# Kernel optimization log

Hardware: AMD Instinct MI355X
Metric: run time of the kernel (lower is better)

The kernel has to match this reference:

```python
import jax, jax.numpy as jnp
import numpy as np

B, S, E, H = 2, 2048, 2048, 16
D = E // H

def setup_inputs() -> dict:
    key = jax.random.key(0)
    ks = jax.random.split(key, 9)
    sc = 1.0 / np.sqrt(E)
    return {
        "x":  jax.random.normal(ks[0], (B, S, E), jnp.float32),
        "Wq": jax.random.normal(ks[1], (E, E), jnp.float32) * sc,
        "bq": jax.random.normal(ks[2], (E,), jnp.float32) * 0.01,
        "Wk": jax.random.normal(ks[3], (E, E), jnp.float32) * sc,
        "bk": jax.random.normal(ks[4], (E,), jnp.float32) * 0.01,
        "Wv": jax.random.normal(ks[5], (E, E), jnp.float32) * sc,
        "bv": jax.random.normal(ks[6], (E,), jnp.float32) * 0.01,
        "Wo": jax.random.normal(ks[7], (E, E), jnp.float32) * sc,
        "bo": jax.random.normal(ks[8], (E,), jnp.float32) * 0.01,
    }

def _split_heads(t):
    # [B,S,E] -> [B,H,S,D]
    return t.reshape(B, S, H, D).transpose(0, 2, 1, 3)

def reference(x, Wq, bq, Wk, bk, Wv, bv, Wo, bo):
    # projections (nn.Linear: y = x @ W^T + b)
    q = _split_heads(x @ Wq.T + bq)
    k = _split_heads(x @ Wk.T + bk)
    v = _split_heads(x @ Wv.T + bv)

    # scaled causal attention; scale uses k.size(-1) == head_dim D
    scores = jnp.einsum("bhqd,bhkd->bhqk", q, k) / jnp.sqrt(jnp.asarray(D, q.dtype))
    causal = jnp.tril(jnp.ones((S, S), bool))  # [S,S]
    scores = jnp.where(causal[None, None, :, :], scores, -jnp.inf)
    # training path subtracts row max before softmax (no-op under stable softmax)
    scores = scores - jnp.max(scores, axis=-1, keepdims=True)
    attn = jax.nn.softmax(scores, axis=-1)
    # dropout_rate = 0.0 -> identity
    ctx = jnp.einsum("bhqk,bhkd->bhqd", attn, v)

    # merge heads [B,H,S,D] -> [B,S,E], final projection
    out = ctx.transpose(0, 2, 1, 3).reshape(B, S, E)
    return out @ Wo.T + bo
```

## Files before the change

kernel.cpp:

```cpp
#include <hip/hip_runtime.h>

typedef unsigned short u16;
typedef __attribute__((ext_vector_type(4))) float f32x4;
typedef __attribute__((ext_vector_type(8))) short s16x8;
typedef __attribute__((ext_vector_type(4))) unsigned short u16x4;
typedef __attribute__((ext_vector_type(2))) unsigned u32x2;

#define MFMA16(a, b, c) __builtin_amdgcn_mfma_f32_16x16x32_bf16((a), (b), (c), 0, 0, 0)

__device__ __forceinline__ u16 f2bf(float f) {
  union { float f; unsigned u; } v; v.f = f;
  unsigned u = v.u;
  u += 0x7fffu + ((u >> 16) & 1u);
  return (u16)(u >> 16);
}

__device__ __forceinline__ unsigned cvtpk(float a, float b) {
  unsigned r;
  asm("v_cvt_pk_bf16_f32 %0, %1, %2" : "=v"(r) : "v"(a), "v"(b));
  return r;
}

__device__ __forceinline__ void gl_lds16(const void* g, void* l) {
  __builtin_amdgcn_global_load_lds(
      (const __attribute__((address_space(1))) void*)g,
      (__attribute__((address_space(3))) void*)l, 16, 0, 0);
}

__global__ void cast6(const float* __restrict__ x,
                      const float* __restrict__ w0, const float* __restrict__ w1,
                      const float* __restrict__ w2, const float* __restrict__ w3,
                      u16* __restrict__ ws) {
  const int y = blockIdx.y;
  const float* src;
  u16* dst;
  if (y < 2) { src = x + (size_t)y * 4194304; dst = ws + (size_t)y * 4194304; }
  else {
    src = (y == 2) ? w0 : (y == 3) ? w1 : (y == 4) ? w2 : w3;
    dst = ws + 8388608 + (size_t)(y - 2) * 4194304;
  }
  const int i = blockIdx.x * 256 + threadIdx.x;
  f32x4 v = ((const f32x4*)src)[i];
  u16x4 o;
#pragma unroll
  for (int e = 0; e < 4; ++e) o[e] = f2bf(v[e]);
  ((u16x4*)dst)[i] = o;
}

template <int SWAP>
__device__ __forceinline__ void gemm_core(const u16* __restrict__ A,
                                          const u16* __restrict__ Bw,
                                          u16* sA, u16* sB,
                                          f32x4 (&acc)[4][4],
                                          int m0, int n0, int tid) {
  const int lane = tid & 63, w = tid >> 6;
  const int ln = lane & 15, quad = lane >> 4, ln7 = ln & 7;
  const int wm = (w >> 1) * 64, wn = (w & 1) * 64;
  const int srow = lane >> 3;
  const int scol = (((lane & 7) ^ srow)) * 8;

  for (int k0 = 0; k0 < 2048; k0 += 64) {
#pragma unroll
    for (int c = 0; c < 4; ++c) {
      const int chunk = c * 4 + w;
      const int row = chunk * 8 + srow;
      gl_lds16(A + (size_t)(m0 + row) * 2048 + k0 + scol, (char*)sA + chunk * 1024);
      gl_lds16(Bw + (size_t)(n0 + row) * 2048 + k0 + scol, (char*)sB + chunk * 1024);
    }
    __syncthreads();
#pragma unroll
    for (int kk = 0; kk < 64; kk += 32) {
      s16x8 af[4], bf[4];
      const int g = (kk >> 3) + quad;
#pragma unroll
      for (int t = 0; t < 4; ++t) {
        af[t] = *(const s16x8*)&sA[(wm + t * 16 + ln) * 64 + ((g ^ ln7) << 3)];
        bf[t] = *(const s16x8*)&sB[(wn + t * 16 + ln) * 64 + ((g ^ ln7) << 3)];
      }
#pragma unroll
      for (int tm = 0; tm < 4; ++tm)
#pragma unroll
        for (int tn = 0; tn < 4; ++tn)
          acc[tm][tn] = SWAP ? MFMA16(bf[tn], af[tm], acc[tm][tn])
                             : MFMA16(af[tm], bf[tn], acc[tm][tn]);
    }
    __syncthreads();
  }
}

__global__ __launch_bounds__(512, 2) void gemm_qk256(
    const u16* __restrict__ A,
    const u16* __restrict__ W0, const u16* __restrict__ W1,
    const float* __restrict__ b0, const float* __restrict__ b1,
    u16* __restrict__ Qo, u16* __restrict__ Ko) {
  __shared__ __align__(16) u16 smem[65536];
  const int z = blockIdx.z;
  const u16* Bw = z ? W1 : W0;
  const float* bias = z ? b1 : b0;
  u16* out = z ? Ko : Qo;
  const float scale = z ? 1.0f : 0.1275174306003988f;

  const int tid = threadIdx.x;
  const int lane = tid & 63, w = tid >> 6;
  const int ln = lane & 15, quad = lane >> 4, ln7 = lane & 7;
  const int m0 = blockIdx.y * 256, n0 = blockIdx.x * 256;
  const int wm = (w >> 2) << 7, wn = (w & 3) << 6;

  const int ci0 = tid, ci1 = 512 + tid;
  const int r0 = ci0 >> 3, c0k = ((ci0 & 7) ^ (r0 & 7)) << 3;
  const int r1 = ci1 >> 3, c1k = ((ci1 & 7) ^ (r1 & 7)) << 3;
  const int abase = (w >> 2) << 13;
  const int bbase = 16384 + (((w >> 1) & 1) << 13) + ((w & 1) << 12);
  const int sw0 = (quad ^ ln7) << 3, sw1 = ((4 + quad) ^ ln7) << 3;

  f32x4 acc[8][4] = {};
  s16x8 af[8][2], bf[4][2];

  auto STGA = [&](int t) {
    u16* dst = smem + ((t & 1) << 15);
    const int kc = (t & 31) << 6;
    const u16* s0 = A + (size_t)(m0 + r0) * 2048 + kc + c0k;
    const u16* s1 = A + (size_t)(m0 + r1) * 2048 + kc + c1k;
    gl_lds16(s0, dst + ci0 * 8);
    gl_lds16(s1, dst + ci1 * 8);
    gl_lds16(s0 + (size_t)128 * 2048, dst + 8192 + ci0 * 8);
    gl_lds16(s1 + (size_t)128 * 2048, dst + 8192 + ci1 * 8);
  };
  auto STGB = [&](int t) {
    u16* dst = smem + ((t & 1) << 15) + 16384;
    const int kc = (t & 31) << 6;
    const u16* s0 = Bw + (size_t)(n0 + r0) * 2048 + kc + c0k;
    const u16* s1 = Bw + (size_t)(n0 + r1) * 2048 + kc + c1k;
    gl_lds16(s0, dst + ci0 * 8);
    gl_lds16(s1, dst + ci1 * 8);
    gl_lds16(s0 + (size_t)128 * 2048, dst + 8192 + ci0 * 8);
    gl_lds16(s1 + (size_t)128 * 2048, dst + 8192 + ci1 * 8);
  };
  auto RDA = [&](int buf, int tm0) {
    const u16* p = smem + (buf << 15) + abase;
#pragma unroll
    for (int u = 0; u < 4; ++u) {
      const int tt = tm0 + u;
      af[tt][0] = *(const s16x8*)&p[(tt * 16 + ln) * 64 + sw0];
      af[tt][1] = *(const s16x8*)&p[(tt * 16 + ln) * 64 + sw1];
    }
  };
  auto RDB = [&](int buf, int tn0) {
    const u16* p = smem + (buf << 15) + bbase;
#pragma unroll
    for (int u = 0; u < 2; ++u) {
      const int tt = tn0 + u;
      bf[tt][0] = *(const s16x8*)&p[(tt * 16 + ln) * 64 + sw0];
      bf[tt][1] = *(const s16x8*)&p[(tt * 16 + ln) * 64 + sw1];
    }
  };
  auto QM = [&](int tm0, int tn0) {
    __builtin_amdgcn_s_setprio(1);
#pragma unroll
    for (int tm = tm0; tm < tm0 + 4; ++tm)
#pragma unroll
      for (int tn = tn0; tn < tn0 + 2; ++tn)
#pragma unroll
        for (int ks = 0; ks < 2; ++ks)
          acc[tm][tn] = MFMA16(bf[tn][ks], af[tm][ks], acc[tm][tn]);
    __builtin_amdgcn_s_setprio(0);
  };

#define BAR()                                   \
  asm volatile("" ::: "memory");                \
  __builtin_amdgcn_s_barrier();                 \
  asm volatile("" ::: "memory")
#define SEAL() asm volatile("s_waitcnt vmcnt(0)" ::: "memory")

  STGA(0); STGB(0); STGA(1);
  asm volatile("s_waitcnt vmcnt(4)" ::: "memory");
  BAR();
  RDA(0, 0); RDB(0, 0);

#pragma unroll 1
  for (int u = 0; u < 16; ++u) {
    const int t = 2 * u;
    QM(0, 0);
    RDA(0, 4);
    STGB(t + 1);
    BAR();
    QM(4, 0);
    RDB(0, 2);
    BAR();
    QM(4, 2);
    SEAL();
    BAR();
    QM(0, 2);
    RDA(1, 0); RDB(1, 0);
    STGA(t + 2);
    BAR();
    QM(0, 0);
    RDA(1, 4);
    STGB(t + 2);
    BAR();
    QM(4, 0);
    RDB(1, 2);
    BAR();
    QM(4, 2);
    SEAL();
    BAR();
    QM(0, 2);
    RDA(0, 0); RDB(0, 0);
    STGA(t + 3);
    BAR();
  }
  asm volatile("s_waitcnt vmcnt(0) lgkmcnt(0)" ::: "memory");
#undef BAR
#undef SEAL

#pragma unroll
  for (int tn = 0; tn < 4; ++tn) {
    const int n_base = n0 + wn + tn * 16 + quad * 4;
    const f32x4 bv = *(const f32x4*)&bias[n_base];
    const int h = n_base >> 7, dl = n_base & 127;
#pragma unroll
    for (int tm = 0; tm < 8; ++tm) {
      const int m = m0 + wm + tm * 16 + ln;
      const int b = m >> 11, s = m & 2047;
      u16x4 ov;
#pragma unroll
      for (int r = 0; r < 4; ++r) ov[r] = f2bf((acc[tm][tn][r] + bv[r]) * scale);
      *(u16x4*)&out[(((size_t)(b * 16 + h)) << 18) + ((size_t)s << 7) + dl] = ov;
    }
  }
}

__global__ __launch_bounds__(256, 2) void gemm_v(const u16* __restrict__ A,
                                                 const u16* __restrict__ Bw,
                                                 const float* __restrict__ bias,
                                                 u16* __restrict__ Vo) {
  __shared__ __align__(16) u16 smem[16384];
  u16* sA = smem;
  u16* sB = smem + 8192;
  const int tid = threadIdx.x;
  const int lane = tid & 63, w = tid >> 6;
  const int ln = lane & 15, quad = lane >> 4;
  const int m0 = blockIdx.y * 128, n0 = blockIdx.x * 128;
  const int wm = (w >> 1) * 64, wn = (w & 1) * 64;

  f32x4 acc[4][4] = {};
  gemm_core<0>(A, Bw, sA, sB, acc, m0, n0, tid);
  const int b = m0 >> 11;
#pragma unroll
  for (int tn = 0; tn < 4; ++tn) {
    const int n = n0 + wn + tn * 16 + ln;
    const float bv = bias[n];
    const int h = n >> 7, dl = n & 127;
#pragma unroll
    for (int tm = 0; tm < 4; ++tm) {
      const int s_base = (m0 & 2047) + wm + tm * 16 + quad * 4;
      u16x4 ov;
#pragma unroll
      for (int r = 0; r < 4; ++r) ov[r] = f2bf(acc[tm][tn][r] + bv);
      *(u16x4*)&Vo[(((size_t)((b * 16 + h) * 128 + dl)) << 11) + s_base] = ov;
    }
  }
}

__global__ __launch_bounds__(256, 2) void gemm_out(const u16* __restrict__ A,
                                                   const u16* __restrict__ Bw,
                                                   const float* __restrict__ bias,
                                                   float* __restrict__ out) {
  __shared__ __align__(16) u16 smem[16384];
  u16* sA = smem;
  u16* sB = smem + 8192;
  const int tid = threadIdx.x;
  const int lane = tid & 63, w = tid >> 6;
  const int ln = lane & 15, quad = lane >> 4;
  const int m0 = blockIdx.y * 128, n0 = blockIdx.x * 128;
  const int wm = (w >> 1) * 64, wn = (w & 1) * 64;

  f32x4 acc[4][4] = {};
  gemm_core<1>(A, Bw, sA, sB, acc, m0, n0, tid);
#pragma unroll
  for (int tn = 0; tn < 4; ++tn) {
    const int n_base = n0 + wn + tn * 16 + quad * 4;
    const f32x4 bv = *(const f32x4*)&bias[n_base];
#pragma unroll
    for (int tm = 0; tm < 4; ++tm) {
      const int m = m0 + wm + tm * 16 + ln;
      f32x4 ov;
#pragma unroll
      for (int r = 0; r < 4; ++r) ov[r] = acc[tm][tn][r] + bv[r];
      *(f32x4*)&out[(size_t)m * 2048 + n_base] = ov;
    }
  }
}

__global__ __launch_bounds__(256, 2) void attn_kernel(const u16* __restrict__ Q,
                                                      const u16* __restrict__ Kp,
                                                      const u16* __restrict__ Vt,
                                                      u16* __restrict__ ctx) {
  __shared__ __align__(16) u16 smem[40960];
  u16* sP = smem;

  const int flat = blockIdx.x + (blockIdx.y << 4);
  const int bh = flat >> 4;
  const int i = (flat < 256) ? (15 - (flat & 15)) : (flat & 15);
  const size_t base = (size_t)bh << 18;

  const int tid = threadIdx.x, lane = tid & 63, w = tid >> 6;
  const int ln = lane & 15, quad = lane >> 4, ln7 = lane & 7;

#pragma unroll
  for (int c = 0; c < 8; ++c) {
    const int chunk0 = (c * 4 + w) * 64;
    const int chunk = chunk0 + lane;
    const int row = chunk >> 4, cc = chunk & 15;
    gl_lds16(Q + base + (size_t)((i * 128 + row) * 128 + ((cc ^ (row & 15)) << 3)),
             (char*)(smem + 8192) + chunk0 * 16);
  }
  __syncthreads();
  s16x8 qf[2][4];
#pragma unroll
  for (int qt = 0; qt < 2; ++qt)
#pragma unroll
    for (int kc = 0; kc < 4; ++kc)
      qf[qt][kc] = *(const s16x8*)&smem[8192 + (w * 32 + qt * 16 + ln) * 128 +
                                        (((kc * 4 + quad) ^ ln) << 3)];
  __syncthreads();

  auto stageK = [&](int j, int buf) {
    u16* dst = smem + 8192 + buf * 8192;
#pragma unroll
    for (int c = 0; c < 4; ++c) {
      const int chunk0 = (c * 4 + w) * 64;
      const int chunk = chunk0 + lane;
      const int row = chunk >> 4, cc = chunk & 15;
      gl_lds16(Kp + base + (size_t)((j * 64 + row) * 128 + ((cc ^ (row & 15)) << 3)),
               (char*)dst + chunk0 * 16);
    }
  };
  auto stageV = [&](int j, int buf) {
    u16* dst = smem + 24576 + buf * 8192;
#pragma unroll
    for (int c = 0; c < 4; ++c) {
      const int chunk0 = (c * 4 + w) * 64;
      const int chunk = chunk0 + lane;
      const int row = chunk >> 3, cc = chunk & 7;
      gl_lds16(Vt + base + (size_t)(row * 2048 + j * 64 + ((cc ^ (row & 7)) << 3)),
               (char*)dst + chunk0 * 16);
    }
  };

  stageK(0, 0);
  stageV(0, 0);
  __syncthreads();

  f32x4 o_acc[8][2] = {};
  float lsum[2] = {0.f, 0.f};
  const int jmax = 2 * i + 1;
  const int qg = i * 128 + w * 32 + ln;

  for (int j = 0; j <= jmax; ++j) {
    const int cb = j & 1;
    if (j < jmax) { stageK(j + 1, cb ^ 1); stageV(j + 1, cb ^ 1); }
    const u16* sK = smem + 8192 + cb * 8192;
    const u16* sV = smem + 24576 + cb * 8192;

    f32x4 sacc[4][2] = {};
#pragma unroll
    for (int kc = 0; kc < 4; ++kc) {
      s16x8 kf[4];
#pragma unroll
      for (int kt = 0; kt < 4; ++kt)
        kf[kt] = *(const s16x8*)&sK[(kt * 16 + ln) * 128 + (((kc * 4 + quad) ^ ln) << 3)];
#pragma unroll
      for (int kt = 0; kt < 4; ++kt)
#pragma unroll
        for (int qt = 0; qt < 2; ++qt)
          sacc[kt][qt] = MFMA16(kf[kt], qf[qt][kc], sacc[kt][qt]);
    }

    const bool diag = (j >= 2 * i);
#pragma unroll
    for (int kt = 0; kt < 4; ++kt)
#pragma unroll
      for (int qt = 0; qt < 2; ++qt) {
        f32x4 pv;
#pragma unroll
        for (int r = 0; r < 4; ++r) {
          float p = __builtin_amdgcn_exp2f(sacc[kt][qt][r]);
          const int kg = j * 64 + kt * 16 + quad * 4 + r;
          if (diag && kg > qg + qt * 16) p = 0.f;
          lsum[qt] += p;
          pv[r] = p;
        }
        u32x2 pk2;
        pk2[0] = cvtpk(pv[0], pv[1]);
        pk2[1] = cvtpk(pv[2], pv[3]);
        const int qrow = w * 32 + qt * 16 + ln;
        const int c = kt * 4 + quad;
        *(u32x2*)&sP[qrow * 64 + ((c ^ (qrow & 14)) << 2)] = pk2;
      }
    asm volatile("s_waitcnt lgkmcnt(0)" ::: "memory");
    __builtin_amdgcn_sched_barrier(0);

#pragma unroll
    for (int kc = 0; kc < 2; ++kc) {
      s16x8 vf[8], pf[2];
#pragma unroll
      for (int qt = 0; qt < 2; ++qt) {
        const int qrow = w * 32 + qt * 16 + ln;
        const int c0 = kc * 8 + quad * 2;
        pf[qt] = *(const s16x8*)&sP[qrow * 64 + ((c0 ^ (qrow & 14)) << 2)];
      }
#pragma unroll
      for (int dt = 0; dt < 8; ++dt)
        vf[dt] = *(const s16x8*)&sV[(dt * 16 + ln) * 64 + (((kc * 4 + quad) ^ ln7) << 3)];
#pragma unroll
      for (int dt = 0; dt < 8; ++dt)
#pragma unroll
        for (int qt = 0; qt < 2; ++qt)
          o_acc[dt][qt] = MFMA16(vf[dt], pf[qt], o_acc[dt][qt]);
    }
    __syncthreads();
  }

  const int b = bh >> 4, h = bh & 15;
  float rinv[2];
#pragma unroll
  for (int qt = 0; qt < 2; ++qt) {
    float s = lsum[qt];
    s += __shfl_xor(s, 16);
    s += __shfl_xor(s, 32);
    rinv[qt] = __builtin_amdgcn_rcpf(s);
  }
#pragma unroll
  for (int dt = 0; dt < 8; ++dt)
#pragma unroll
    for (int qt = 0; qt < 2; ++qt) {
      const int sg = i * 128 + w * 32 + qt * 16 + ln;
      const int d0 = h * 128 + dt * 16 + quad * 4;
      u16x4 ov;
#pragma unroll
      for (int r = 0; r < 4; ++r) ov[r] = f2bf(o_acc[dt][qt][r] * rinv[qt]);
      *(u16x4*)&ctx[((size_t)b << 22) + (size_t)sg * 2048 + d0] = ov;
    }
}

extern "C" void kernel_launch(void* const* d_in, const int* in_sizes, int n_in,
                              void* d_out, int out_size, void* d_ws, size_t ws_size,
                              hipStream_t stream) {
  const float* x = (const float*)d_in[0];
  const float* Wq = (const float*)d_in[1];
  const float* bq = (const float*)d_in[2];
  const float* Wk = (const float*)d_in[3];
  const float* bk = (const float*)d_in[4];
  const float* Wv = (const float*)d_in[5];
  const float* bv = (const float*)d_in[6];
  const float* Wo = (const float*)d_in[7];
  const float* bo = (const float*)d_in[8];

  u16* ws = (u16*)d_ws;
  u16* xb = ws;
  u16* Wqb = xb + 8388608;
  u16* Wkb = Wqb + 4194304;
  u16* Wvb = Wkb + 4194304;
  u16* Wob = Wvb + 4194304;
  u16* Qb = Wob + 4194304;
  u16* Kb = Qb + 8388608;
  u16* Vtb = Kb + 8388608;
  u16* ctxb = Vtb + 8388608;

  cast6<<<dim3(4096, 6), 256, 0, stream>>>(x, Wq, Wk, Wv, Wo, ws);

  gemm_qk256<<<dim3(8, 16, 2), 512, 0, stream>>>(xb, Wqb, Wkb, bq, bk, Qb, Kb);
  gemm_v<<<dim3(16, 32), 256, 0, stream>>>(xb, Wvb, bv, Vtb);

  attn_kernel<<<dim3(16, 32), 256, 0, stream>>>(Qb, Kb, Vtb, ctxb);

  gemm_out<<<dim3(16, 32), 256, 0, stream>>>(ctxb, Wob, bo, (float*)d_out);
}
```

Before: 349.9 us.

## Simplify QK GEMM pipeline and double-buffer V/out GEMMs with 256x128 tiles

Replaces the hand-interleaved QK GEMM schedule, which had many barriers per iteration, with a simpler double-buffered loop: one wait and one barrier per K-step, with the next tile prefetched before compute. The V and output projection GEMMs move from single-buffered 128x128 tiles with 256 threads to double-buffered 256x128 tiles with 512 threads, so global-to-LDS loads overlap MFMA work. The aim is less barrier overhead and hidden load latency in the GEMMs. In exchange, QK loses its fine-grained interleave of LDS reads and MFMAs, and the V/out kernels use more LDS per block, which may reduce occupancy.

Measured after the change: 339.9 us. 1.03x faster.

```diff
diff --git a/kernel.cpp b/kernel.cpp
--- a/kernel.cpp
+++ b/kernel.cpp
@@ -26,6 +26,11 @@
       (const __attribute__((address_space(1))) void*)g,
       (__attribute__((address_space(3))) void*)l, 16, 0, 0);
 }
+
+#define BARF()                                  \
+  asm volatile("" ::: "memory");                \
+  __builtin_amdgcn_s_barrier();                 \
+  asm volatile("" ::: "memory")
 
 __global__ void cast6(const float* __restrict__ x,
                       const float* __restrict__ w0, const float* __restrict__ w1,
@@ -47,47 +52,6 @@
   ((u16x4*)dst)[i] = o;
 }
 
-template <int SWAP>
-__device__ __forceinline__ void gemm_core(const u16* __restrict__ A,
-                                          const u16* __restrict__ Bw,
-                                          u16* sA, u16* sB,
-                                          f32x4 (&acc)[4][4],
-                                          int m0, int n0, int tid) {
-  const int lane = tid & 63, w = tid >> 6;
-  const int ln = lane & 15, quad = lane >> 4, ln7 = ln & 7;
-  const int wm = (w >> 1) * 64, wn = (w & 1) * 64;
-  const int srow = lane >> 3;
-  const int scol = (((lane & 7) ^ srow)) * 8;
-
-  for (int k0 = 0; k0 < 2048; k0 += 64) {
-#pragma unroll
-    for (int c = 0; c < 4; ++c) {
-      const int chunk = c * 4 + w;
-      const int row = chunk * 8 + srow;
-      gl_lds16(A + (size_t)(m0 + row) * 2048 + k0 + scol, (char*)sA + chunk * 1024);
-      gl_lds16(Bw + (size_t)(n0 + row) * 2048 + k0 + scol, (char*)sB + chunk * 1024);
-    }
-    __syncthreads();
-#pragma unroll
-    for (int kk = 0; kk < 64; kk += 32) {
-      s16x8 af[4], bf[4];
-      const int g = (kk >> 3) + quad;
-#pragma unroll
-      for (int t = 0; t < 4; ++t) {
-        af[t] = *(const s16x8*)&sA[(wm + t * 16 + ln) * 64 + ((g ^ ln7) << 3)];
-        bf[t] = *(const s16x8*)&sB[(wn + t * 16 + ln) * 64 + ((g ^ ln7) << 3)];
-      }
-#pragma unroll
-      for (int tm = 0; tm < 4; ++tm)
-#pragma unroll
-        for (int tn = 0; tn < 4; ++tn)
-          acc[tm][tn] = SWAP ? MFMA16(bf[tn], af[tm], acc[tm][tn])
-                             : MFMA16(af[tm], bf[tn], acc[tm][tn]);
-    }
-    __syncthreads();
-  }
-}
-
 __global__ __launch_bounds__(512, 2) void gemm_qk256(
     const u16* __restrict__ A,
     const u16* __restrict__ W0, const u16* __restrict__ W1,
@@ -106,11 +70,10 @@
   const int m0 = blockIdx.y * 256, n0 = blockIdx.x * 256;
   const int wm = (w >> 2) << 7, wn = (w & 3) << 6;
 
-  const int ci0 = tid, ci1 = 512 + tid;
-  const int r0 = ci0 >> 3, c0k = ((ci0 & 7) ^ (r0 & 7)) << 3;
-  const int r1 = ci1 >> 3, c1k = ((ci1 & 7) ^ (r1 & 7)) << 3;
-  const int abase = (w >> 2) << 13;
-  const int bbase = 16384 + (((w >> 1) & 1) << 13) + ((w & 1) << 12);
+  const int r0 = tid >> 3;
+  const int ck = ((tid & 7) ^ (r0 & 7)) << 3;
+  const int abase = wm * 64;
+  const int bbase = 16384 + wn * 64;
   const int sw0 = (quad ^ ln7) << 3, sw1 = ((4 + quad) ^ ln7) << 3;
 
   f32x4 acc[8][4] = {};
@@ -118,23 +81,19 @@
 
   auto STGA = [&](int t) {
     u16* dst = smem + ((t & 1) << 15);
-    const int kc = (t & 31) << 6;
-    const u16* s0 = A + (size_t)(m0 + r0) * 2048 + kc + c0k;
-    const u16* s1 = A + (size_t)(m0 + r1) * 2048 + kc + c1k;
-    gl_lds16(s0, dst + ci0 * 8);
-    gl_lds16(s1, dst + ci1 * 8);
-    gl_lds16(s0 + (size_t)128 * 2048, dst + 8192 + ci0 * 8);
-    gl_lds16(s1 + (size_t)128 * 2048, dst + 8192 + ci1 * 8);
+    const int kc = t << 6;
+    const u16* s0 = A + (size_t)(m0 + r0) * 2048 + kc + ck;
+#pragma unroll
+    for (int g = 0; g < 4; ++g)
+      gl_lds16(s0 + (size_t)(g * 64) * 2048, dst + g * 4096 + tid * 8);
   };
   auto STGB = [&](int t) {
     u16* dst = smem + ((t & 1) << 15) + 16384;
-    const int kc = (t & 31) << 6;
-    const u16* s0 = Bw + (size_t)(n0 + r0) * 2048 + kc + c0k;
-    const u16* s1 = Bw + (size_t)(n0 + r1) * 2048 + kc + c1k;
-    gl_lds16(s0, dst + ci0 * 8);
-    gl_lds16(s1, dst + ci1 * 8);
-    gl_lds16(s0 + (size_t)128 * 2048, dst + 8192 + ci0 * 8);
-    gl_lds16(s1 + (size_t)128 * 2048, dst + 8192 + ci1 * 8);
+    const int kc = t << 6;
+    const u16* s0 = Bw + (size_t)(n0 + r0) * 2048 + kc + ck;
+#pragma unroll
+    for (int g = 0; g < 4; ++g)
+      gl_lds16(s0 + (size_t)(g * 64) * 2048, dst + g * 4096 + tid * 8);
   };
   auto RDA = [&](int buf, int tm0) {
     const u16* p = smem + (buf << 15) + abase;
@@ -166,52 +125,22 @@
     __builtin_amdgcn_s_setprio(0);
   };
 
-#define BAR()                                   \
-  asm volatile("" ::: "memory");                \
-  __builtin_amdgcn_s_barrier();                 \
-  asm volatile("" ::: "memory")
-#define SEAL() asm volatile("s_waitcnt vmcnt(0)" ::: "memory")
-
-  STGA(0); STGB(0); STGA(1);
-  asm volatile("s_waitcnt vmcnt(4)" ::: "memory");
-  BAR();
-  RDA(0, 0); RDB(0, 0);
-
+  STGA(0); STGB(0);
 #pragma unroll 1
-  for (int u = 0; u < 16; ++u) {
-    const int t = 2 * u;
+  for (int t = 0; t < 32; ++t) {
+    const int cb = t & 1;
+    asm volatile("s_waitcnt vmcnt(0)" ::: "memory");
+    BARF();
+    if (t < 31) { STGA(t + 1); STGB(t + 1); }
+    RDA(cb, 0); RDB(cb, 0);
     QM(0, 0);
-    RDA(0, 4);
-    STGB(t + 1);
-    BAR();
+    RDA(cb, 4);
     QM(4, 0);
-    RDB(0, 2);
-    BAR();
+    RDB(cb, 2);
     QM(4, 2);
-    SEAL();
-    BAR();
     QM(0, 2);
-    RDA(1, 0); RDB(1, 0);
-    STGA(t + 2);
-    BAR();
-    QM(0, 0);
-    RDA(1, 4);
-    STGB(t + 2);
-    BAR();
-    QM(4, 0);
-    RDB(1, 2);
-    BAR();
-    QM(4, 2);
-    SEAL();
-    BAR();
-    QM(0, 2);
-    RDA(0, 0); RDB(0, 0);
-    STGA(t + 3);
-    BAR();
   }
   asm volatile("s_waitcnt vmcnt(0) lgkmcnt(0)" ::: "memory");
-#undef BAR
-#undef SEAL
 
 #pragma unroll
   for (int tn = 0; tn < 4; ++tn) {
@@ -230,21 +159,78 @@
   }
 }
 
-__global__ __launch_bounds__(256, 2) void gemm_v(const u16* __restrict__ A,
+template <int SWAP>
+__device__ __forceinline__ void gemm1b_n128(const u16* __restrict__ A,
+                                            const u16* __restrict__ Bw,
+                                            u16* smem, f32x4 (&acc)[4][4],
+                                            int m0, int n0, int tid) {
+  const int lane = tid & 63, w = tid >> 6;
+  const int ln = lane & 15, quad = lane >> 4, ln7 = lane & 7;
+  const int wm = (w >> 1) * 64, wn = (w & 1) * 64;
+  const int r0 = tid >> 3;
+  const int ck = ((tid & 7) ^ (r0 & 7)) << 3;
+  const int sw0 = (quad ^ ln7) << 3, sw1 = ((4 + quad) ^ ln7) << 3;
+
+  s16x8 af[4][2], bf[4][2];
+
+  auto STG = [&](int t) {
+    u16* dst = smem + (t & 1) * 24576;
+    const int kc = t << 6;
+    const u16* sa = A + (size_t)(m0 + r0) * 2048 + kc + ck;
+#pragma unroll
+    for (int g = 0; g < 4; ++g)
+      gl_lds16(sa + (size_t)(g * 64) * 2048, dst + g * 4096 + tid * 8);
+    const u16* sb = Bw + (size_t)(n0 + r0) * 2048 + kc + ck;
+#pragma unroll
+    for (int g = 0; g < 2; ++g)
+      gl_lds16(sb + (size_t)(g * 64) * 2048, dst + 16384 + g * 4096 + tid * 8);
+  };
+  auto RD = [&](int buf) {
+    const u16* pa = smem + buf * 24576 + wm * 64;
+    const u16* pb = smem + buf * 24576 + 16384 + wn * 64;
+#pragma unroll
+    for (int tt = 0; tt < 4; ++tt) {
+      af[tt][0] = *(const s16x8*)&pa[(tt * 16 + ln) * 64 + sw0];
+      af[tt][1] = *(const s16x8*)&pa[(tt * 16 + ln) * 64 + sw1];
+      bf[tt][0] = *(const s16x8*)&pb[(tt * 16 + ln) * 64 + sw0];
+      bf[tt][1] = *(const s16x8*)&pb[(tt * 16 + ln) * 64 + sw1];
+    }
+  };
+
+  STG(0);
+#pragma unroll 1
+  for (int t = 0; t < 32; ++t) {
+    asm volatile("s_waitcnt vmcnt(0)" ::: "memory");
+    BARF();
+    if (t < 31) STG(t + 1);
+    RD(t & 1);
+    __builtin_amdgcn_s_setprio(1);
+#pragma unroll
+    for (int tm = 0; tm < 4; ++tm)
+#pragma unroll
+      for (int tn = 0; tn < 4; ++tn)
+#pragma unroll
+        for (int ks = 0; ks < 2; ++ks)
+          acc[tm][tn] = SWAP ? MFMA16(bf[tn][ks], af[tm][ks], acc[tm][tn])
+                             : MFMA16(af[tm][ks], bf[tn][ks], acc[tm][tn]);
+    __builtin_amdgcn_s_setprio(0);
+  }
+  asm volatile("s_waitcnt vmcnt(0) lgkmcnt(0)" ::: "memory");
+}
+
+__global__ __launch_bounds__(512, 2) void gemm_v(const u16* __restrict__ A,
                                                  const u16* __restrict__ Bw,
                                                  const float* __restrict__ bias,
                                                  u16* __restrict__ Vo) {
-  __shared__ __align__(16) u16 smem[16384];
-  u16* sA = smem;
-  u16* sB = smem + 8192;
+  __shared__ __align__(16) u16 smem[49152];
   const int tid = threadIdx.x;
   const int lane = tid & 63, w = tid >> 6;
   const int ln = lane & 15, quad = lane >> 4;
-  const int m0 = blockIdx.y * 128, n0 = blockIdx.x * 128;
+  const int m0 = blockIdx.y * 256, n0 = blockIdx.x * 128;
   const int wm = (w >> 1) * 64, wn = (w & 1) * 64;
 
   f32x4 acc[4][4] = {};
-  gemm_core<0>(A, Bw, sA, sB, acc, m0, n0, tid);
+  gemm1b_n128<0>(A, Bw, smem, acc, m0, n0, tid);
   const int b = m0 >> 11;
 #pragma unroll
   for (int tn = 0; tn < 4; ++tn) {
@@ -262,21 +248,19 @@
   }
 }
 
-__global__ __launch_bounds__(256, 2) void gemm_out(const u16* __restrict__ A,
+__global__ __launch_bounds__(512, 2) void gemm_out(const u16* __restrict__ A,
                                                    const u16* __restrict__ Bw,
                                                    const float* __restrict__ bias,
                                                    float* __restrict__ out) {
-  __shared__ __align__(16) u16 smem[16384];
-  u16* sA = smem;
-  u16* sB = smem + 8192;
+  __shared__ __align__(16) u16 smem[49152];
   const int tid = threadIdx.x;
   const int lane = tid & 63, w = tid >> 6;
   const int ln = lane & 15, quad = lane >> 4;
-  const int m0 = blockIdx.y * 128, n0 = blockIdx.x * 128;
+  const int m0 = blockIdx.y * 256, n0 = blockIdx.x * 128;
   const int wm = (w >> 1) * 64, wn = (w & 1) * 64;
 
   f32x4 acc[4][4] = {};
-  gemm_core<1>(A, Bw, sA, sB, acc, m0, n0, tid);
+  gemm1b_n128<1>(A, Bw, smem, acc, m0, n0, tid);
 #pragma unroll
   for (int tn = 0; tn < 4; ++tn) {
     const int n_base = n0 + wn + tn * 16 + quad * 4;
@@ -471,9 +455,9 @@
   cast6<<<dim3(4096, 6), 256, 0, stream>>>(x, Wq, Wk, Wv, Wo, ws);
 
   gemm_qk256<<<dim3(8, 16, 2), 512, 0, stream>>>(xb, Wqb, Wkb, bq, bk, Qb, Kb);
-  gemm_v<<<dim3(16, 32), 256, 0, stream>>>(xb, Wvb, bv, Vtb);
+  gemm_v<<<dim3(16, 16), 512, 0, stream>>>(xb, Wvb, bv, Vtb);
 
   attn_kernel<<<dim3(16, 32), 256, 0, stream>>>(Qb, Kb, Vtb, ctxb);
 
-  gemm_out<<<dim3(16, 32), 256, 0, stream>>>(ctxb, Wob, bo, (float*)d_out);
-}
+  gemm_out<<<dim3(16, 16), 512, 0, stream>>>(ctxb, Wob, bo, (float*)d_out);
+}
```
